# Performance work log

Hardware: AMD Instinct MI355X
Metric: run time of the kernel (lower is better)

## Reference

```python
import jax, jax.numpy as jnp
import numpy as np
from jax import lax

EPSILON = 1e-12


def _sobel_kernels(n1=1, n2=2, n3=2):
    Sx = np.asarray([[[-n1, 0, n1], [-n2, 0, n2], [-n1, 0, n1]],
                     [[-n2, 0, n2], [-n3 * n2, 0, n3 * n2], [-n2, 0, n2]],
                     [[-n1, 0, n1], [-n2, 0, n2], [-n1, 0, n1]]])
    Sy = np.asarray([[[-n1, -n2, -n1], [0, 0, 0], [n1, n2, n1]],
                     [[-n2, -n3 * n2, -n2], [0, 0, 0], [n2, n3 * n2, n2]],
                     [[-n1, -n2, -n1], [0, 0, 0], [n1, n2, n1]]])
    Sz = np.asarray([[[-n1, -n2, -n1], [-n2, -n3 * n2, -n2], [-n1, -n2, -n1]],
                     [[0, 0, 0], [0, 0, 0], [0, 0, 0]],
                     [[n1, n2, n1], [n2, n3 * n2, n2], [n1, n2, n1]]])
    Sd11 = np.asarray([[[0, n1, n2], [-n1, 0, n1], [-n2, -n1, 0]],
                       [[0, n2, n2 * n3], [-n2, 0, n2], [-n2 * n3, -n2, 0]],
                       [[0, n1, n2], [-n1, 0, n1], [-n2, -n1, 0]]])
    Sd12 = np.asarray([[[-n2, -n1, 0], [-n1, 0, n1], [0, n1, n2]],
                       [[-n2 * n3, -n2, 0], [-n2, 0, n2], [0, n2, n2 * n3]],
                       [[-n2, -n1, 0], [-n1, 0, n1], [0, n1, n2]]])
    Sd21 = Sd11.T
    Sd22 = Sd12.T
    Sd31 = np.asarray([-S.T for S in Sd11.T])
    Sd32 = np.asarray([S.T for S in Sd12.T])
    ks = np.stack([Sx, Sy, Sz, Sd11, Sd12, Sd21, Sd22, Sd31, Sd32]).astype(np.float32)
    return jnp.asarray(ks[:, None])  # [9, 1, 3, 3, 3] (OIDHW)


_KERNELS = _sobel_kernels(1, 2, 2)


def _edge_magnitude(img):
    # img: [B, C, H, W, D]. Per-channel convs are summed over C in the original;
    # by linearity of conv, sum channels first, then run all 9 stencils at once.
    C = img.shape[1]
    x = jnp.sum(img, axis=1, keepdims=True)  # [B, 1, H, W, D]
    g = lax.conv_general_dilated(
        x, _KERNELS, window_strides=(1, 1, 1), padding='SAME',
        dimension_numbers=('NCDHW', 'OIDHW', 'NCDHW'))  # [B, 9, H, W, D]
    mag = jnp.sqrt(jnp.sum(g * g, axis=1, keepdims=True) + EPSILON)
    return mag / C  # (1/C) * sqrt(sum_sq + eps), matches operator precedence


def setup_inputs() -> dict:
    key = jax.random.key(0)
    k1, k2 = jax.random.split(key)
    shape = (2, 2, 128, 128, 128)
    y = jax.random.normal(k1, shape, dtype=jnp.float32)
    yp = jax.random.normal(k2, shape, dtype=jnp.float32)
    return {"y": y, "yp": yp}


def reference(y, yp):
    y_edge = _edge_magnitude(y)
    yp_edge = _edge_magnitude(yp)
    return jnp.mean((y_edge - yp_edge) ** 2)  # nn.MSELoss default 'mean'
```

## Files before the change

### kernel.cpp

```cpp
#include <hip/hip_runtime.h>


namespace {

constexpr int ZDIM = 128, YDIM = 128, XDIM = 128;
constexpr int TX = 32;
constexpr int TY = 8;
constexpr int ZC = 16;
constexpr int LW = TX + 2;
constexpr int PLANE = (TY + 2) * LW;
constexpr float INV_N = 1.0f / 4194304.0f;

__global__ void zero_out_kernel(float* out) { *out = 0.0f; }

__device__ __forceinline__ void plane_combos(const float* __restrict__ s,
                                             int ty, int tx, float* __restrict__ C) {
    float sx[3], dx[3], ex[3];
#pragma unroll
    for (int r = 0; r < 3; ++r) {
        const float a0 = s[(ty + r) * LW + tx + 0];
        const float a1 = s[(ty + r) * LW + tx + 1];
        const float a2 = s[(ty + r) * LW + tx + 2];
        const float t = a0 + a2;
        ex[r] = t + a1;
        sx[r] = t + 2.0f * a1;
        dx[r] = a2 - a0;
    }
    C[0] = dx[0] + 2.0f * dx[1] + dx[2];
    C[1] = sx[2] - sx[0];
    C[2] = sx[0] + 2.0f * sx[1] + sx[2];
    C[3] = dx[0] + dx[1] + dx[2];
    C[4] = ex[2] - ex[0];
    C[5] = sx[0] + sx[1] + sx[2];
    C[6] = ex[0] + 2.0f * ex[1] + ex[2];
}

__device__ __forceinline__ float edge_mag_half(const float* __restrict__ Ca,
                                               const float* __restrict__ Cb,
                                               const float* __restrict__ Cc) {
    const float g1  = Ca[0] + 2.0f * Cb[0] + Cc[0];
    const float g2  = Ca[1] + 2.0f * Cb[1] + Cc[1];
    const float g3  = Cc[2] - Ca[2];
    const float Azx = Ca[3] + 2.0f * Cb[3] + Cc[3];
    const float Azy = Ca[4] + 2.0f * Cb[4] + Cc[4];
    const float Axz = Cc[5] - Ca[5];
    const float Axy = Ca[1] + Cb[1] + Cc[1];
    const float Ayx = Ca[0] + Cb[0] + Cc[0];
    const float Ayz = Cc[6] - Ca[6];
    const float g4 = Azx - Azy, g5 = Azx + Azy;
    const float g6 = Axz - Axy, g7 = Axz + Axy;
    const float g8 = Ayx - Ayz, g9 = Ayx + Ayz;
    const float ssq = g1 * g1 + g2 * g2 + g3 * g3 + g4 * g4 + g5 * g5
                    + g6 * g6 + g7 * g7 + g8 * g8 + g9 * g9;
    return 0.5f * sqrtf(ssq + 1e-12f);
}

__global__ __launch_bounds__(TX * TY)
void gme_loss_kernel(const float* __restrict__ y,
                     const float* __restrict__ yp,
                     float* __restrict__ out) {
    const int tx = threadIdx.x;
    const int ty = threadIdx.y;
    const int tid = ty * TX + tx;

    const int bx = blockIdx.x;
    const int x0 = (bx & 3) * TX;
    const int y0 = (bx >> 2) * TY;
    const int z0 = blockIdx.y * ZC;
    const int b  = blockIdx.z;

    const int gy = y0 + ty;

    __shared__ float sY[PLANE];
    __shared__ float sP[PLANE];
    __shared__ float red[4];

    const size_t cstride = (size_t)ZDIM * YDIM * XDIM;
    const size_t bbase   = (size_t)b * 2 * cstride;

    float CaY[7], CbY[7], CaP[7], CbP[7];
#pragma unroll
    for (int i = 0; i < 7; ++i) { CaY[i] = 0.f; CbY[i] = 0.f; CaP[i] = 0.f; CbP[i] = 0.f; }

    float acc = 0.0f;

    for (int zc = z0 - 1; zc <= z0 + ZC; ++zc) {
        __syncthreads();
        if (zc >= 0 && zc < ZDIM) {
            const size_t zrow = bbase + (size_t)zc * YDIM * XDIM;
            for (int i = tid; i < PLANE; i += TX * TY) {
                const int ly = i / LW;
                const int lx = i - ly * LW;
                const int py = y0 - 1 + ly;
                const int px = x0 - 1 + lx;
                float vy = 0.0f, vp = 0.0f;
                if (py >= 0 && py < YDIM && px >= 0 && px < XDIM) {
                    const size_t idx = zrow + (size_t)py * XDIM + px;
                    vy = y[idx]  + y[idx + cstride];
                    vp = yp[idx] + yp[idx + cstride];
                }
                sY[i] = vy;
                sP[i] = vp;
            }
        } else {
            for (int i = tid; i < PLANE; i += TX * TY) { sY[i] = 0.f; sP[i] = 0.f; }
        }
        __syncthreads();

        float CcY[7], CcP[7];
        plane_combos(sY, ty, tx, CcY);
        plane_combos(sP, ty, tx, CcP);

        if (zc >= z0 + 1) {
            const float my = edge_mag_half(CaY, CbY, CcY);
            const float mp = edge_mag_half(CaP, CbP, CcP);
            const float d = my - mp;
            acc += d * d;
        }

#pragma unroll
        for (int i = 0; i < 7; ++i) {
            CaY[i] = CbY[i]; CbY[i] = CcY[i];
            CaP[i] = CbP[i]; CbP[i] = CcP[i];
        }
        (void)gy;
    }

#pragma unroll
    for (int off = 32; off > 0; off >>= 1) acc += __shfl_down(acc, off);
    const int lane = tid & 63;
    const int wave = tid >> 6;
    if (lane == 0) red[wave] = acc;
    __syncthreads();
    if (tid == 0) {
        const float s = (red[0] + red[1] + red[2] + red[3]) * INV_N;
        atomicAdd(out, s);
    }
}

}

extern "C" void kernel_launch(void* const* d_in, const int* in_sizes, int n_in,
                              void* d_out, int out_size, void* d_ws, size_t ws_size,
                              hipStream_t stream) {
    const float* y  = (const float*)d_in[0];
    const float* yp = (const float*)d_in[1];
    float* out = (float*)d_out;

    zero_out_kernel<<<1, 1, 0, stream>>>(out);

    dim3 block(TX, TY, 1);
    dim3 grid((XDIM / TX) * (YDIM / TY),
              ZDIM / ZC,
              2);
    gme_loss_kernel<<<grid, block, 0, stream>>>(y, yp, out);
}
```

Before: 127.7 us.

## Double-buffer LDS planes with register prefetch and float4 halo loads

Each z-plane's halo tile is now loaded with float4 global reads by a fixed set of slot threads, with the row width padded to 40. The next plane is prefetched into registers while the current one is computed, and shared memory is double-buffered so each step needs a single barrier. The plane combos are kept in a rotating three-slot register ring instead of being copied each step, and the arithmetic is rewritten with FMAs and reused partial sums. The wider halo loads fetch extra edge columns and raise register pressure, and the zeroing kernel is replaced with hipMemsetAsync.

```diff
diff --git a/kernel.cpp b/kernel.cpp
--- a/kernel.cpp
+++ b/kernel.cpp
@@ -4,138 +4,155 @@
 namespace {
 
 constexpr int ZDIM = 128, YDIM = 128, XDIM = 128;
-constexpr int TX = 32;
-constexpr int TY = 8;
-constexpr int ZC = 16;
-constexpr int LW = TX + 2;
-constexpr int PLANE = (TY + 2) * LW;
+constexpr int TX = 32, TY = 8, ZC = 16;
+constexpr int LW = 40;
+constexpr int ROWS = TY + 2;
+constexpr int PLANE = ROWS * LW;
+constexpr int QPR = LW / 4;
+constexpr int NSLOT = ROWS * QPR;
+constexpr int YX = YDIM * XDIM;
+constexpr size_t CS = (size_t)ZDIM * YX;
 constexpr float INV_N = 1.0f / 4194304.0f;
 
-__global__ void zero_out_kernel(float* out) { *out = 0.0f; }
-
-__device__ __forceinline__ void plane_combos(const float* __restrict__ s,
-                                             int ty, int tx, float* __restrict__ C) {
-    float sx[3], dx[3], ex[3];
+__device__ __forceinline__ void plane_combos(const float* __restrict__ p,
+                                             float* __restrict__ C) {
+  float sx[3], dx[3], ex[3];
 #pragma unroll
-    for (int r = 0; r < 3; ++r) {
-        const float a0 = s[(ty + r) * LW + tx + 0];
-        const float a1 = s[(ty + r) * LW + tx + 1];
-        const float a2 = s[(ty + r) * LW + tx + 2];
-        const float t = a0 + a2;
-        ex[r] = t + a1;
-        sx[r] = t + 2.0f * a1;
-        dx[r] = a2 - a0;
-    }
-    C[0] = dx[0] + 2.0f * dx[1] + dx[2];
-    C[1] = sx[2] - sx[0];
-    C[2] = sx[0] + 2.0f * sx[1] + sx[2];
-    C[3] = dx[0] + dx[1] + dx[2];
-    C[4] = ex[2] - ex[0];
-    C[5] = sx[0] + sx[1] + sx[2];
-    C[6] = ex[0] + 2.0f * ex[1] + ex[2];
+  for (int r = 0; r < 3; ++r) {
+    const float a0 = p[r * LW + 0];
+    const float a1 = p[r * LW + 1];
+    const float a2 = p[r * LW + 2];
+    const float t = a0 + a2;
+    ex[r] = t + a1;
+    sx[r] = __builtin_fmaf(2.0f, a1, t);
+    dx[r] = a2 - a0;
+  }
+  C[3] = (dx[0] + dx[2]) + dx[1];
+  C[0] = C[3] + dx[1];
+  C[1] = sx[2] - sx[0];
+  C[5] = (sx[0] + sx[2]) + sx[1];
+  C[2] = C[5] + sx[1];
+  C[4] = ex[2] - ex[0];
+  C[6] = __builtin_fmaf(2.0f, ex[1], ex[0] + ex[2]);
 }
 
 __device__ __forceinline__ float edge_mag_half(const float* __restrict__ Ca,
                                                const float* __restrict__ Cb,
                                                const float* __restrict__ Cc) {
-    const float g1  = Ca[0] + 2.0f * Cb[0] + Cc[0];
-    const float g2  = Ca[1] + 2.0f * Cb[1] + Cc[1];
-    const float g3  = Cc[2] - Ca[2];
-    const float Azx = Ca[3] + 2.0f * Cb[3] + Cc[3];
-    const float Azy = Ca[4] + 2.0f * Cb[4] + Cc[4];
-    const float Axz = Cc[5] - Ca[5];
-    const float Axy = Ca[1] + Cb[1] + Cc[1];
-    const float Ayx = Ca[0] + Cb[0] + Cc[0];
-    const float Ayz = Cc[6] - Ca[6];
-    const float g4 = Azx - Azy, g5 = Azx + Azy;
-    const float g6 = Axz - Axy, g7 = Axz + Axy;
-    const float g8 = Ayx - Ayz, g9 = Ayx + Ayz;
-    const float ssq = g1 * g1 + g2 * g2 + g3 * g3 + g4 * g4 + g5 * g5
-                    + g6 * g6 + g7 * g7 + g8 * g8 + g9 * g9;
-    return 0.5f * sqrtf(ssq + 1e-12f);
+  const float g1  = __builtin_fmaf(2.0f, Cb[0], Ca[0] + Cc[0]);
+  const float g2  = __builtin_fmaf(2.0f, Cb[1], Ca[1] + Cc[1]);
+  const float g3  = Cc[2] - Ca[2];
+  const float Azx = __builtin_fmaf(2.0f, Cb[3], Ca[3] + Cc[3]);
+  const float Azy = __builtin_fmaf(2.0f, Cb[4], Ca[4] + Cc[4]);
+  const float Axz = Cc[5] - Ca[5];
+  const float Axy = g2 - Cb[1];
+  const float Ayx = g1 - Cb[0];
+  const float Ayz = Cc[6] - Ca[6];
+  const float g4 = Azx - Azy, g5 = Azx + Azy;
+  const float g6 = Axz - Axy, g7 = Axz + Axy;
+  const float g8 = Ayx - Ayz, g9 = Ayx + Ayz;
+  float s = __builtin_fmaf(g1, g1, 1e-12f);
+  s = __builtin_fmaf(g2, g2, s); s = __builtin_fmaf(g3, g3, s);
+  s = __builtin_fmaf(g4, g4, s); s = __builtin_fmaf(g5, g5, s);
+  s = __builtin_fmaf(g6, g6, s); s = __builtin_fmaf(g7, g7, s);
+  s = __builtin_fmaf(g8, g8, s); s = __builtin_fmaf(g9, g9, s);
+  return 0.5f * sqrtf(s);
 }
 
-__global__ __launch_bounds__(TX * TY)
+__global__ __launch_bounds__(256)
 void gme_loss_kernel(const float* __restrict__ y,
                      const float* __restrict__ yp,
                      float* __restrict__ out) {
-    const int tx = threadIdx.x;
-    const int ty = threadIdx.y;
-    const int tid = ty * TX + tx;
+  const int tx  = threadIdx.x;
+  const int ty  = threadIdx.y;
+  const int tid = ty * TX + tx;
 
-    const int bx = blockIdx.x;
-    const int x0 = (bx & 3) * TX;
-    const int y0 = (bx >> 2) * TY;
-    const int z0 = blockIdx.y * ZC;
-    const int b  = blockIdx.z;
+  const int bx = blockIdx.x;
+  const int x0 = (bx & 3) * TX;
+  const int y0 = (bx >> 2) * TY;
+  const int z0 = blockIdx.y * ZC;
+  const int b  = blockIdx.z;
 
-    const int gy = y0 + ty;
+  __shared__ __align__(16) float lds[2][2][PLANE];
+  __shared__ float red[4];
 
-    __shared__ float sY[PLANE];
-    __shared__ float sP[PLANE];
-    __shared__ float red[4];
+  const bool has_slot = tid < 2 * NSLOT;
+  bool sok = false;
+  const float* gp = nullptr;
+  float* w0 = nullptr; float* w1 = nullptr;
+  if (has_slot) {
+    const int vol = tid >= NSLOT;
+    const int s   = tid - vol * NSLOT;
+    const int ly  = s / QPR;
+    const int lx  = s - ly * QPR;
+    const int py  = y0 - 1 + ly;
+    const int px  = x0 - 4 + 4 * lx;
+    sok = (py >= 0) & (py < YDIM) & (px >= 0) & (px <= XDIM - 4);
+    const float* src = vol ? yp : y;
+    gp = src + (size_t)b * 2 * CS + (size_t)py * XDIM + px;
+    w0 = &lds[vol][0][ly * LW + lx * 4];
+    w1 = &lds[vol][1][ly * LW + lx * 4];
+  }
 
-    const size_t cstride = (size_t)ZDIM * YDIM * XDIM;
-    const size_t bbase   = (size_t)b * 2 * cstride;
+  const int ridx = ty * LW + tx + 3;
+  const float* rY0 = &lds[0][0][ridx];
+  const float* rY1 = &lds[0][1][ridx];
+  const float* rP0 = &lds[1][0][ridx];
+  const float* rP1 = &lds[1][1][ridx];
 
-    float CaY[7], CbY[7], CaP[7], CbP[7];
-#pragma unroll
-    for (int i = 0; i < 7; ++i) { CaY[i] = 0.f; CbY[i] = 0.f; CaP[i] = 0.f; CbP[i] = 0.f; }
+  auto prefetch = [&](int zc) -> float4 {
+    float4 v = make_float4(0.f, 0.f, 0.f, 0.f);
+    if (sok && (unsigned)zc < (unsigned)ZDIM) {
+      const float* p = gp + (size_t)zc * YX;
+      const float4 a = *(const float4*)p;
+      const float4 c = *(const float4*)(p + CS);
+      v.x = a.x + c.x; v.y = a.y + c.y; v.z = a.z + c.z; v.w = a.w + c.w;
+    }
+    return v;
+  };
 
-    float acc = 0.0f;
+  float KY[3][7] = {}, KP[3][7] = {};
+  float acc = 0.0f;
 
-    for (int zc = z0 - 1; zc <= z0 + ZC; ++zc) {
-        __syncthreads();
-        if (zc >= 0 && zc < ZDIM) {
-            const size_t zrow = bbase + (size_t)zc * YDIM * XDIM;
-            for (int i = tid; i < PLANE; i += TX * TY) {
-                const int ly = i / LW;
-                const int lx = i - ly * LW;
-                const int py = y0 - 1 + ly;
-                const int px = x0 - 1 + lx;
-                float vy = 0.0f, vp = 0.0f;
-                if (py >= 0 && py < YDIM && px >= 0 && px < XDIM) {
-                    const size_t idx = zrow + (size_t)py * XDIM + px;
-                    vy = y[idx]  + y[idx + cstride];
-                    vp = yp[idx] + yp[idx + cstride];
-                }
-                sY[i] = vy;
-                sP[i] = vp;
-            }
-        } else {
-            for (int i = tid; i < PLANE; i += TX * TY) { sY[i] = 0.f; sP[i] = 0.f; }
-        }
-        __syncthreads();
+  float4 pf = prefetch(z0 - 1);
 
-        float CcY[7], CcP[7];
-        plane_combos(sY, ty, tx, CcY);
-        plane_combos(sP, ty, tx, CcP);
+#pragma unroll 6
+  for (int i = 0; i < ZC + 2; ++i) {
+    const int zc = z0 - 1 + i;
+    if (has_slot) {
+      float* w = (i & 1) ? w1 : w0;
+      *(float4*)w = pf;
+    }
+    if (i < ZC + 1) pf = prefetch(zc + 1);
+    __syncthreads();
 
-        if (zc >= z0 + 1) {
-            const float my = edge_mag_half(CaY, CbY, CcY);
-            const float mp = edge_mag_half(CaP, CbP, CcP);
-            const float d = my - mp;
-            acc += d * d;
-        }
+    float* Cc_y = KY[i % 3];
+    float* Cc_p = KP[i % 3];
+    plane_combos((i & 1) ? rY1 : rY0, Cc_y);
+    plane_combos((i & 1) ? rP1 : rP0, Cc_p);
+
+    if (i >= 2) {
+      const float* Ca_y = KY[(i + 1) % 3];
+      const float* Cb_y = KY[(i + 2) % 3];
+      const float* Ca_p = KP[(i + 1) % 3];
+      const float* Cb_p = KP[(i + 2) % 3];
+      const float my = edge_mag_half(Ca_y, Cb_y, Cc_y);
+      const float mp = edge_mag_half(Ca_p, Cb_p, Cc_p);
+      const float d = my - mp;
+      acc = __builtin_fmaf(d, d, acc);
+    }
+  }
 
 #pragma unroll
-        for (int i = 0; i < 7; ++i) {
-            CaY[i] = CbY[i]; CbY[i] = CcY[i];
-            CaP[i] = CbP[i]; CbP[i] = CcP[i];
-        }
-        (void)gy;
-    }
-
-#pragma unroll
-    for (int off = 32; off > 0; off >>= 1) acc += __shfl_down(acc, off);
-    const int lane = tid & 63;
-    const int wave = tid >> 6;
-    if (lane == 0) red[wave] = acc;
-    __syncthreads();
-    if (tid == 0) {
-        const float s = (red[0] + red[1] + red[2] + red[3]) * INV_N;
-        atomicAdd(out, s);
-    }
+  for (int off = 32; off > 0; off >>= 1) acc += __shfl_down(acc, off);
+  const int lane = tid & 63;
+  const int wave = tid >> 6;
+  if (lane == 0) red[wave] = acc;
+  __syncthreads();
+  if (tid == 0) {
+    const float s = (red[0] + red[1] + red[2] + red[3]) * INV_N;
+    atomicAdd(out, s);
+  }
 }
 
 }
@@ -143,15 +160,15 @@
 extern "C" void kernel_launch(void* const* d_in, const int* in_sizes, int n_in,
                               void* d_out, int out_size, void* d_ws, size_t ws_size,
                               hipStream_t stream) {
-    const float* y  = (const float*)d_in[0];
-    const float* yp = (const float*)d_in[1];
-    float* out = (float*)d_out;
+  const float* y  = (const float*)d_in[0];
+  const float* yp = (const float*)d_in[1];
+  float* out = (float*)d_out;
 
-    zero_out_kernel<<<1, 1, 0, stream>>>(out);
+  hipMemsetAsync(out, 0, sizeof(float), stream);
 
-    dim3 block(TX, TY, 1);
-    dim3 grid((XDIM / TX) * (YDIM / TY),
-              ZDIM / ZC,
-              2);
-    gme_loss_kernel<<<grid, block, 0, stream>>>(y, yp, out);
+  dim3 block(TX, TY, 1);
+  dim3 grid((XDIM / TX) * (YDIM / TY),
+            ZDIM / ZC,
+            2);
+  gme_loss_kernel<<<grid, block, 0, stream>>>(y, yp, out);
 }
```

New measurement: 122.1 us. 4.3% less time.
